# Performance work log

Measured on AMD Instinct MI355X. Metric: run time of the kernel, lower is better.

Reference implementation:

```python
import jax, jax.numpy as jnp
import numpy as np

B, N, K, CIN, COUT, H = 4, 2048, 32, 16, 32, 32
EPS = 1e-5


def setup_inputs() -> dict:
    key = jax.random.key(0)
    ks = jax.random.split(key, 6)
    s = 0.1
    return dict(
        xyz=jax.random.uniform(ks[0], (B, N, 3), dtype=jnp.float32),
        points=jax.random.normal(ks[1], (B, N, CIN), dtype=jnp.float32),
        W1=jax.random.normal(ks[2], (3, H), dtype=jnp.float32) * s,
        b1=jnp.zeros((H,), jnp.float32),
        g1=jnp.ones((H,), jnp.float32),
        be1=jnp.zeros((H,), jnp.float32),
        W2=jax.random.normal(ks[3], (H, H), dtype=jnp.float32) * s,
        b2=jnp.zeros((H,), jnp.float32),
        g2=jnp.ones((H,), jnp.float32),
        be2=jnp.zeros((H,), jnp.float32),
        W3=jax.random.normal(ks[4], (H, CIN * COUT), dtype=jnp.float32) * s,
        b3=jnp.zeros((CIN * COUT,), jnp.float32),
        gbn=jnp.ones((COUT,), jnp.float32),
        bbn=jnp.zeros((COUT,), jnp.float32),
    )


def _bn(h, g, b):
    # BatchNorm1d training-mode math: biased batch stats over axis 0
    return g * (h - h.mean(0)) / jnp.sqrt(h.var(0) + EPS) + b


def reference(xyz, points, W1, b1, g1, be1, W2, b2, g2, be2, W3, b3, gbn, bbn):
    # KNN: squared distances (B,N,N)
    sq = jnp.sum(xyz * xyz, -1)
    dist = -2.0 * jnp.einsum('bmc,bnc->bmn', xyz, xyz) + sq[:, :, None] + sq[:, None, :]
    _, idx = jax.lax.top_k(-dist, K)  # (B,N,K) nearest neighbors

    gather = jax.vmap(lambda p, i: p[i])  # (N,C),(N,K)->(N,K,C), vmapped over B
    grouped_xyz = gather(xyz, idx)                      # (B,N,K,3)
    rel = grouped_xyz - xyz[:, :, None, :]              # (B,N,K,3)
    grouped_pts = gather(points, idx)                   # (B,N,K,CIN)

    # weight net on relative coords
    h = rel.reshape(-1, 3)
    h = _bn(jax.nn.relu(h @ W1 + b1), g1, be1)
    h = _bn(jax.nn.relu(h @ W2 + b2), g2, be2)
    w = (h @ W3 + b3).reshape(B, N, K, CIN, COUT)       # (B,N,K,CIN,COUT)

    # weighted sum over C_in, then max over neighbors
    out = jnp.einsum('bnkc,bnkco->bnko', grouped_pts, w)  # (B,N,K,COUT)
    out = out.max(axis=2)                                 # (B,N,COUT)

    # final BatchNorm1d over (B,N) per channel
    m = out.mean((0, 1))
    v = out.var((0, 1))
    return gbn * (out - m) / jnp.sqrt(v + EPS) + bbn
```

## Files before the change

### kernel.cpp

```cpp
#include <hip/hip_runtime.h>

#define B_ 4
#define N_ 2048
#define K_ 32
#define CIN_ 16
#define COUT_ 32
#define H_ 32
#define R_ (B_*N_*K_)
#define EPS_ 1e-5f
#define INVR_ (1.0f/(float)R_)
#define INVBN_ (1.0f/(float)(B_*N_))
#define LISTCAP 112
#define NSH 16

typedef __attribute__((ext_vector_type(8)))  _Float16 f16x8;
typedef __attribute__((ext_vector_type(2)))  __fp16   hw16x2;
typedef __attribute__((ext_vector_type(2)))  _Float16 f16x2;
typedef __attribute__((ext_vector_type(16))) float    f32x16;

__device__ __forceinline__ float dot3f(float ax,float ay,float az,float bx,float by,float bz){
    return fmaf(az,bz, fmaf(ay,by, ax*bx));
}
__device__ __forceinline__ unsigned int pk2(float a, float b){
    union { hw16x2 v; unsigned int u; } c;
    c.v = __builtin_amdgcn_cvt_pkrtz(a, b);
    return c.u;
}
__device__ __forceinline__ unsigned int pkmul(unsigned int a, unsigned int b){
    union { unsigned int u; f16x2 v; } x, y, r;
    x.u = a; y.u = b; r.v = x.v * y.v; return r.u;
}
__device__ __forceinline__ float shsum(const float* __restrict__ p, int k){
    float s = 0.f;
    #pragma unroll
    for (int i = 0; i < NSH; ++i) s += p[i*32 + k];
    return s;
}

__global__ __launch_bounds__(256) void k_prep0(const float* __restrict__ xyz, float4* __restrict__ xs4g,
                                               float* __restrict__ st){
    int i = blockIdx.x*256 + threadIdx.x;
    float x = xyz[3*i], y = xyz[3*i+1], z = xyz[3*i+2];
    xs4g[i] = make_float4(x, y, z, dot3f(x,y,z,x,y,z));
    if (blockIdx.x == 0){
        for (int j = threadIdx.x; j < 1152; j += 256) st[j] = 0.f;
    }
}

__global__ __launch_bounds__(256,6) void k_knn(const float4* __restrict__ xs4g,
                                               const float* __restrict__ W1, const float* __restrict__ b1,
                                               int* __restrict__ idx_out,
                                               float* __restrict__ s1sh, float* __restrict__ q1sh){
    __shared__ unsigned int hist[4][512][2];
    __shared__ unsigned long long lst[4][LISTCAP];
    __shared__ int kidx[4][K_];

    const int tid  = threadIdx.x;
    const int w    = tid >> 6;
    const int lane = tid & 63;
    const int half = lane >> 5;
    const int b    = blockIdx.x >> 9;
    const int q    = ((blockIdx.x & 511) << 2) + w;
    const int bN   = b * N_;
    unsigned int* hw = &hist[w][0][0];

    const uint4 z4 = make_uint4(0,0,0,0);
    uint4* h4 = (uint4*)hw;
    #pragma unroll
    for (int i = 0; i < 4; ++i) h4[i*64 + lane] = z4;

    const float4 qp = xs4g[bN + q];
    const float qx = qp.x, qy = qp.y, qz = qp.z, sqq = qp.w;

    unsigned int fv[32];
    #pragma unroll
    for (int j = 0; j < 32; ++j){
        int c = j*64 + lane;
        float4 pt = xs4g[bN + c];
        float d = fmaf(-2.0f, dot3f(qx,qy,qz, pt.x,pt.y,pt.z), sqq) + pt.w;
        fv[j] = __float_as_uint(d);
        unsigned int u1 = __float_as_uint(d + 1.0f);
        unsigned int key = (u1 <= 0x3F800000u) ? 0u : ((u1 - 0x3F800000u) >> 15);
        key = key > 511u ? 511u : key;
        atomicAdd(&hw[key*2 + (lane & 1)], 1u);
    }

    unsigned int g[8];
    #pragma unroll
    for (int t = 0; t < 4; ++t){
        uint4 h = ((const uint4*)hw)[lane*4 + t];
        g[2*t]   = h.x + h.y;
        g[2*t+1] = h.z + h.w;
    }
    unsigned int gs = 0;
    #pragma unroll
    for (int t = 0; t < 8; ++t) gs += g[t];
    unsigned int cum = gs;
    #pragma unroll
    for (int off = 1; off < 64; off <<= 1){
        unsigned int v = __shfl_up(cum, off);
        if (lane >= off) cum += v;
    }
    unsigned long long bal = __ballot(cum >= (unsigned)K_);
    int L = __ffsll(bal) - 1;
    unsigned int run = __shfl(cum, L) - __shfl(gs, L);
    int Bsel = 8*L + 7;
    {
        unsigned int c = run; bool fnd = false;
        #pragma unroll
        for (int t = 0; t < 8; ++t){
            unsigned int ht = __shfl(g[t], L, 64);
            if (!fnd && c + ht >= (unsigned)K_){ Bsel = 8*L + t; fnd = true; }
            c += ht;
        }
    }
    const float Tedge = __uint_as_float(0x3F800000u + ((unsigned)(Bsel + 1) << 15));
    const bool allin = (Bsel == 511);

    const unsigned long long mlt = (lane == 63) ? ~0ull >> 1 : (1ull << lane) - 1ull;
    unsigned int cnt = 0;
    #pragma unroll
    for (int j = 0; j < 32; ++j){
        float f1 = __uint_as_float(fv[j]) + 1.0f;
        bool surv = (f1 < Tedge) || allin;
        unsigned long long sb = __ballot(surv);
        unsigned int pos = cnt + (unsigned int)__popcll(sb & mlt);
        if (surv && pos < (unsigned)LISTCAP)
            lst[w][pos] = ((unsigned long long)fv[j] << 32) | (unsigned int)(j*64 + lane);
        cnt += (unsigned int)__popcll(sb);
    }
    int m = (int)cnt; if (m > LISTCAP) m = LISTCAP;

    int* outp = idx_out + ((size_t)bN + q) * K_;
    for (int i = lane; i < m; i += 64){
        unsigned long long my = lst[w][i];
        int rank = 0;
        for (int jj = 0; jj < m; ++jj)
            rank += (lst[w][jj] < my) ? 1 : 0;
        if (rank < K_){
            int id = (int)(unsigned int)(my & 0xFFFFFFFFull);
            outp[rank] = id;
            kidx[w][rank] = id;
        }
    }

    {
        const int ch = lane & 31;
        float w1a = W1[ch], w1b = W1[H_+ch], w1c = W1[2*H_+ch], b1c = b1[ch];
        float s = 0.f, qq = 0.f;
        #pragma unroll
        for (int r = 0; r < 16; ++r){
            int idr = kidx[w][half*16 + r];
            float4 pn = xs4g[bN + idr];
            float rx = pn.x - qx, ry = pn.y - qy, rz = pn.z - qz;
            float h = fmaxf(fmaf(rx, w1a, fmaf(ry, w1b, fmaf(rz, w1c, b1c))), 0.0f);
            s += h; qq = fmaf(h, h, qq);
        }
        s  += __shfl_xor(s, 32, 64);
        qq += __shfl_xor(qq, 32, 64);
        if (lane < 32){
            int sh = (blockIdx.x & (NSH-1)) * 32 + ch;
            atomicAdd(&s1sh[sh], s);
            atomicAdd(&q1sh[sh], qq);
        }
    }
}

__device__ __forceinline__ void compute_h1v(const float4* __restrict__ xs4g, const int* __restrict__ idx, int r,
                                            const float* __restrict__ W1, const float* __restrict__ b1, float* h1){
    int b = r >> 16;
    int n = (r >> 5) & (N_-1);
    int id = idx[r];
    float4 pc = xs4g[b*N_ + n];
    float4 pn = xs4g[b*N_ + id];
    float rx = pn.x - pc.x, ry = pn.y - pc.y, rz = pn.z - pc.z;
    #pragma unroll
    for (int j = 0; j < H_; ++j){
        float a = fmaf(rx, W1[j], fmaf(ry, W1[H_+j], fmaf(rz, W1[2*H_+j], b1[j])));
        h1[j] = fmaxf(a, 0.0f);
    }
}

__global__ __launch_bounds__(256) void k_prep2(const float* __restrict__ points,
                                               const float* __restrict__ s1s, const float* __restrict__ q1s,
                                               const float* __restrict__ g1, const float* __restrict__ be1,
                                               const float* __restrict__ W2, const float* __restrict__ b2,
                                               unsigned int* __restrict__ pf16, unsigned int* __restrict__ W2f,
                                               float* __restrict__ b2p){
    int flat = blockIdx.x*256 + threadIdx.x;
    if (flat < 65536){
        pf16[flat] = pk2(points[2*flat], points[2*flat+1]);
    } else if (flat < 66048){
        int d = flat - 65536;
        int jj = d & 3, lane = (d >> 2) & 63, s = d >> 8;
        int col = lane & 31;
        int k0 = s*16 + (lane >> 5)*8 + 2*jj;
        float m0 = shsum(s1s,k0)*INVR_,   v0 = shsum(q1s,k0)*INVR_   - m0*m0;
        float m1 = shsum(s1s,k0+1)*INVR_, v1 = shsum(q1s,k0+1)*INVR_ - m1*m1;
        float a0  = g1[k0]   / sqrtf(v0 + EPS_);
        float a1v = g1[k0+1] / sqrtf(v1 + EPS_);
        W2f[d] = pk2(a0*W2[k0*H_ + col], a1v*W2[(k0+1)*H_ + col]);
    } else if (flat < 66080){
        int col = flat - 66048;
        float acc = b2[col];
        #pragma unroll 4
        for (int h = 0; h < H_; ++h){
            float mm = shsum(s1s,h)*INVR_, vv = shsum(q1s,h)*INVR_ - mm*mm;
            float aa = g1[h] / sqrtf(vv + EPS_);
            float bb = fmaf(-aa, mm, be1[h]);
            acc = fmaf(bb, W2[h*H_ + col], acc);
        }
        b2p[col] = acc;
    }
}

__global__ __launch_bounds__(256,4) void k_h2stats(const float4* __restrict__ xs4g, const int* __restrict__ idx,
                                                   const float* __restrict__ W1, const float* __restrict__ b1,
                                                   const uint4* __restrict__ W2f, const float* __restrict__ b2p,
                                                   float* gsum, float* gsq){
    __shared__ float redS[H_], redQ[H_];
    const int tid = threadIdx.x, lane = tid & 63, w = tid >> 6;
    const int half = lane >> 5, m = lane & 31;
    if (tid < H_){ redS[tid] = 0.f; redQ[tid] = 0.f; }
    __syncthreads();

    int r = blockIdx.x*256 + tid;
    float h1[H_];
    compute_h1v(xs4g, idx, r, W1, b1, h1);
    unsigned int h1p[16];
    #pragma unroll
    for (int i = 0; i < 16; ++i) h1p[i] = pk2(h1[2*i], h1[2*i+1]);

    union { uint4 u4; f16x8 v; } Bf0, Bf1;
    Bf0.u4 = W2f[lane];
    Bf1.u4 = W2f[64 + lane];
    float b2c = b2p[m];

    float s = 0.f, q = 0.f;
    #pragma unroll
    for (int t = 0; t < 2; ++t){
        const int src = t*32 + m;
        union { unsigned int u[4]; f16x8 v; } a0, a1f;
        #pragma unroll
        for (int jj = 0; jj < 4; ++jj){
            unsigned int lo = __shfl(h1p[jj],     src, 64);
            unsigned int hi = __shfl(h1p[4 + jj], src, 64);
            a0.u[jj] = half ? hi : lo;
        }
        #pragma unroll
        for (int jj = 0; jj < 4; ++jj){
            unsigned int lo = __shfl(h1p[8 + jj],  src, 64);
            unsigned int hi = __shfl(h1p[12 + jj], src, 64);
            a1f.u[jj] = half ? hi : lo;
        }
        f32x16 acc;
        #pragma unroll
        for (int i = 0; i < 16; ++i) acc[i] = b2c;
        acc = __builtin_amdgcn_mfma_f32_32x32x16_f16(a0.v,  Bf0.v, acc, 0, 0, 0);
        acc = __builtin_amdgcn_mfma_f32_32x32x16_f16(a1f.v, Bf1.v, acc, 0, 0, 0);
        #pragma unroll
        for (int i = 0; i < 16; ++i){
            float v = fmaxf(acc[i], 0.0f);
            s += v; q = fmaf(v, v, q);
        }
    }
    s += __shfl_xor(s, 32, 64);
    q += __shfl_xor(q, 32, 64);
    if (lane < 32){ atomicAdd(&redS[m], s); atomicAdd(&redQ[m], q); }
    __syncthreads();
    if (tid < H_){ atomicAdd(&gsum[tid], redS[tid]); atomicAdd(&gsq[tid], redQ[tid]); }
}

__global__ __launch_bounds__(256) void k_prep3(const float* __restrict__ W3, const float* __restrict__ b3,
                                               const float* __restrict__ s2, const float* __restrict__ q2,
                                               const float* __restrict__ g2, const float* __restrict__ be2,
                                               unsigned int* __restrict__ W3f){
    int d = blockIdx.x*256 + threadIdx.x;
    int jj = d & 3, lane = (d >> 2) & 63, step = d >> 8;
    int col = lane & 31;
    int off = (lane >> 5)*8 + 2*jj;
    float v0, v1;
    if (step < 32){
        int h = step, c0 = off;
        float mm = s2[h]*INVR_, vv = q2[h]*INVR_ - mm*mm;
        float aa = g2[h] / sqrtf(vv + EPS_);
        v0 = aa * W3[h*512 + c0*COUT_ + col];
        v1 = aa * W3[h*512 + (c0+1)*COUT_ + col];
    } else {
        int c0 = off;
        v0 = b3[c0*COUT_ + col]; v1 = b3[(c0+1)*COUT_ + col];
        #pragma unroll 4
        for (int h = 0; h < H_; ++h){
            float mm = s2[h]*INVR_, vv = q2[h]*INVR_ - mm*mm;
            float aa = g2[h] / sqrtf(vv + EPS_);
            float bb = fmaf(-aa, mm, be2[h]);
            v0 = fmaf(bb, W3[h*512 + c0*COUT_ + col], v0);
            v1 = fmaf(bb, W3[h*512 + (c0+1)*COUT_ + col], v1);
        }
    }
    W3f[d] = pk2(v0, v1);
}

__global__ __launch_bounds__(256,3) void k_out(const float4* __restrict__ xs4g, const int* __restrict__ idx,
                                               const float* __restrict__ W1, const float* __restrict__ b1,
                                               const uint4* __restrict__ W2f, const float* __restrict__ b2p,
                                               const unsigned int* __restrict__ pf16,
                                               const uint4* __restrict__ W3f,
                                               float* __restrict__ out_pre, float* gsum, float* gsq){
    __shared__ float redS[COUT_], redQ[COUT_];
    const int tid = threadIdx.x, lane = tid & 63, w = tid >> 6;
    const int half = lane >> 5, m = lane & 31;
    if (tid < COUT_){ redS[tid] = 0.f; redQ[tid] = 0.f; }
    __syncthreads();

    const int rB = blockIdx.x*256 + w*64;
    int r = blockIdx.x*256 + tid;

    float h1[H_];
    compute_h1v(xs4g, idx, r, W1, b1, h1);
    unsigned int h1p[16];
    #pragma unroll
    for (int i = 0; i < 16; ++i) h1p[i] = pk2(h1[2*i], h1[2*i+1]);

    union { uint4 u4; f16x8 v; } A0, A1;
    A0.u4 = W2f[lane];
    A1.u4 = W2f[64 + lane];
    float b2v[16];
    #pragma unroll
    for (int i = 0; i < 16; ++i) b2v[i] = b2p[(i&3) + 8*(i>>2) + 4*half];

    const uint4* Wf = W3f + lane;

    #pragma unroll
    for (int t = 0; t < 2; ++t){
        const int src = t*32 + m;
        union { unsigned int u[4]; f16x8 v; } B0f, B1f;
        #pragma unroll
        for (int jj = 0; jj < 4; ++jj){
            unsigned int lo = __shfl(h1p[jj],     src, 64);
            unsigned int hi = __shfl(h1p[4 + jj], src, 64);
            B0f.u[jj] = half ? hi : lo;
        }
        #pragma unroll
        for (int jj = 0; jj < 4; ++jj){
            unsigned int lo = __shfl(h1p[8 + jj],  src, 64);
            unsigned int hi = __shfl(h1p[12 + jj], src, 64);
            B1f.u[jj] = half ? hi : lo;
        }
        f32x16 c2;
        #pragma unroll
        for (int i = 0; i < 16; ++i) c2[i] = b2v[i];
        c2 = __builtin_amdgcn_mfma_f32_32x32x16_f16(A0.v, B0f.v, c2, 0, 0, 0);
        c2 = __builtin_amdgcn_mfma_f32_32x32x16_f16(A1.v, B1f.v, c2, 0, 0, 0);

        unsigned int h2p[16];
        #pragma unroll
        for (int p = 0; p < 8; ++p){
            float v0 = fmaxf(c2[2*p],   0.0f);
            float v1 = fmaxf(c2[2*p+1], 0.0f);
            unsigned int ow = pk2(v0, v1);
            unsigned int ot = __shfl_xor(ow, 32, 64);
            int a = p >> 1, bb = p & 1;
            h2p[4*a + 2*half     + bb] = ow;
            h2p[4*a + 2*(1-half) + bb] = ot;
        }

        int row = rB + t*32 + m;
        int bb_ = row >> 16;
        int idr = idx[row];
        const uint4* gpp = (const uint4*)(pf16 + ((size_t)bb_*N_ + idr)*8);
        uint4 ga = gpp[0], gb = gpp[1];
        unsigned int gsel[4];
        gsel[0] = half ? gb.x : ga.x;
        gsel[1] = half ? gb.y : ga.y;
        gsel[2] = half ? gb.z : ga.z;
        gsel[3] = half ? gb.w : ga.w;

        f32x16 acc;
        #pragma unroll
        for (int i = 0; i < 16; ++i) acc[i] = 0.f;
        #pragma unroll
        for (int kb = 0; kb < 32; ++kb){
            unsigned int hr = h2p[kb >> 1];
            unsigned int hd = __builtin_amdgcn_perm(hr, hr, (kb & 1) ? 0x03020302u : 0x01000100u);
            union { unsigned int u[4]; f16x8 v; } af;
            #pragma unroll
            for (int jj = 0; jj < 4; ++jj) af.u[jj] = pkmul(hd, gsel[jj]);
            union { uint4 u4; f16x8 v; } bf; bf.u4 = Wf[kb*64];
            acc = __builtin_amdgcn_mfma_f32_32x32x16_f16(af.v, bf.v, acc, 0, 0, 0);
        }
        {
            union { unsigned int u[4]; f16x8 v; } af;
            #pragma unroll
            for (int jj = 0; jj < 4; ++jj) af.u[jj] = gsel[jj];
            union { uint4 u4; f16x8 v; } bf; bf.u4 = Wf[32*64];
            acc = __builtin_amdgcn_mfma_f32_32x32x16_f16(af.v, bf.v, acc, 0, 0, 0);
        }

        float v = acc[0];
        #pragma unroll
        for (int i = 1; i < 16; ++i) v = fmaxf(v, acc[i]);
        v = fmaxf(v, __shfl_xor(v, 32, 64));
        if (lane < 32){
            int g = blockIdx.x*8 + w*2 + t;
            out_pre[(size_t)g*COUT_ + m] = v;
            atomicAdd(&redS[m], v);
            atomicAdd(&redQ[m], v*v);
        }
    }
    __syncthreads();
    if (tid < COUT_){ atomicAdd(&gsum[tid], redS[tid]); atomicAdd(&gsq[tid], redQ[tid]); }
}

__global__ __launch_bounds__(256) void k_bn(const float* __restrict__ out_pre,
                                            const float* __restrict__ s3, const float* __restrict__ q3,
                                            const float* __restrict__ gbn, const float* __restrict__ bbn,
                                            float* __restrict__ out){
    int i = blockIdx.x*256 + threadIdx.x;
    int o = i & (COUT_-1);
    float mm = s3[o] * INVBN_;
    float vv = q3[o] * INVBN_ - mm*mm;
    float aa = gbn[o] / sqrtf(vv + EPS_);
    out[i] = fmaf(aa, out_pre[i], fmaf(-aa, mm, bbn[o]));
}

extern "C" void kernel_launch(void* const* d_in, const int* in_sizes, int n_in,
                              void* d_out, int out_size, void* d_ws, size_t ws_size,
                              hipStream_t stream){
    const float* xyz    = (const float*)d_in[0];
    const float* points = (const float*)d_in[1];
    const float* W1  = (const float*)d_in[2];
    const float* b1  = (const float*)d_in[3];
    const float* g1  = (const float*)d_in[4];
    const float* be1 = (const float*)d_in[5];
    const float* W2  = (const float*)d_in[6];
    const float* b2  = (const float*)d_in[7];
    const float* g2  = (const float*)d_in[8];
    const float* be2 = (const float*)d_in[9];
    const float* W3  = (const float*)d_in[10];
    const float* b3  = (const float*)d_in[11];
    const float* gbn = (const float*)d_in[12];
    const float* bbn = (const float*)d_in[13];
    float* out = (float*)d_out;

    char* base = (char*)d_ws;
    int*            idx     = (int*)(base + 0);
    float*          out_pre = (float*)(base + 1048576);
    unsigned int*   pf16    = (unsigned int*)(base + 2097152);
    unsigned int*   W3f     = (unsigned int*)(base + 2359296);
    unsigned int*   W2f     = (unsigned int*)(base + 2393088);
    float*          b2p     = (float*)(base + 2395136);
    float*          st      = (float*)(base + 2395264);
    float4*         xs4g    = (float4*)(base + 2399872);
    float *s1s=st, *q1s=st+512, *s2=st+1024, *q2=st+1056, *s3=st+1088, *q3=st+1120;

    hipLaunchKernelGGL(k_prep0,   dim3(32),      dim3(256), 0, stream, xyz, xs4g, st);
    hipLaunchKernelGGL(k_knn,     dim3(B_*N_/4), dim3(256), 0, stream, xs4g, W1, b1, idx, s1s, q1s);
    hipLaunchKernelGGL(k_prep2,   dim3(260),     dim3(256), 0, stream, points, s1s, q1s, g1, be1, W2, b2,
                       pf16, W2f, b2p);
    hipLaunchKernelGGL(k_h2stats, dim3(R_/256),  dim3(256), 0, stream, xs4g, idx, W1, b1,
                       (const uint4*)W2f, b2p, s2, q2);
    hipLaunchKernelGGL(k_prep3,   dim3(33),      dim3(256), 0, stream, W3, b3, s2, q2, g2, be2, W3f);
    hipLaunchKernelGGL(k_out,     dim3(R_/256),  dim3(256), 0, stream, xs4g, idx, W1, b1,
                       (const uint4*)W2f, b2p, pf16, (const uint4*)W3f, out_pre, s3, q3);
    hipLaunchKernelGGL(k_bn,      dim3(B_*N_*COUT_/256), dim3(256), 0, stream, out_pre, s3, q3, gbn, bbn, out);
}
```

Baseline: 176.1 us.

## Fuse all pipeline stages into one cooperative persistent kernel with grid syncs

Replaces the seven separate kernel launches with a single cooperative kernel. Each former kernel becomes a grid-strided phase separated by grid.sync(). The aim is to remove per-launch overhead and inter-kernel gaps, and the small prep kernels now run on the full grid. In exchange it adds six grid-wide barriers. Occupancy is capped by the launch bounds and the union of shared-memory needs, which may slow the heavy KNN and MFMA phases compared with their tuned standalone launches.

```diff
diff --git a/kernel.cpp b/kernel.cpp
--- a/kernel.cpp
+++ b/kernel.cpp
@@ -1,4 +1,7 @@
 #include <hip/hip_runtime.h>
+#include <hip/hip_cooperative_groups.h>
+
+namespace cg = cooperative_groups;
 
 #define B_ 4
 #define N_ 2048
@@ -37,391 +40,398 @@
     return s;
 }
 
-__global__ __launch_bounds__(256) void k_prep0(const float* __restrict__ xyz, float4* __restrict__ xs4g,
-                                               float* __restrict__ st){
-    int i = blockIdx.x*256 + threadIdx.x;
-    float x = xyz[3*i], y = xyz[3*i+1], z = xyz[3*i+2];
-    xs4g[i] = make_float4(x, y, z, dot3f(x,y,z,x,y,z));
-    if (blockIdx.x == 0){
-        for (int j = threadIdx.x; j < 1152; j += 256) st[j] = 0.f;
-    }
-}
-
-__global__ __launch_bounds__(256,6) void k_knn(const float4* __restrict__ xs4g,
-                                               const float* __restrict__ W1, const float* __restrict__ b1,
-                                               int* __restrict__ idx_out,
-                                               float* __restrict__ s1sh, float* __restrict__ q1sh){
-    __shared__ unsigned int hist[4][512][2];
-    __shared__ unsigned long long lst[4][LISTCAP];
-    __shared__ int kidx[4][K_];
+union SharedMem {
+    struct {
+        unsigned int hist[4][512][2];
+        unsigned long long lst[4][LISTCAP];
+        int kidx[4][K_];
+    } knn;
+    struct {
+        float redS[32], redQ[32];
+    } red;
+};
+
+__global__ __launch_bounds__(256,3) void k_mega(
+        const float* __restrict__ xyz, const float* __restrict__ points,
+        const float* __restrict__ W1, const float* __restrict__ b1,
+        const float* __restrict__ g1, const float* __restrict__ be1,
+        const float* __restrict__ W2, const float* __restrict__ b2,
+        const float* __restrict__ g2, const float* __restrict__ be2,
+        const float* __restrict__ W3, const float* __restrict__ b3,
+        const float* __restrict__ gbn, const float* __restrict__ bbn,
+        float* __restrict__ out, char* __restrict__ base)
+{
+    cg::grid_group grid = cg::this_grid();
+
+    int*            idx     = (int*)(base);
+    float*          out_pre = (float*)(base + 1048576);
+    unsigned int*   pf16    = (unsigned int*)(base + 2097152);
+    unsigned int*   W3f     = (unsigned int*)(base + 2359296);
+    float*          st      = (float*)(base + 2393088);
+    float4*         xs4g    = (float4*)(base + 2398208);
+    unsigned int*   W2fg    = (unsigned int*)(base + 2529280);
+    float*          b2pg    = (float*)(base + 2531328);
+    float *s1s = st, *q1s = st+512, *s2 = st+1024, *q2 = st+1056, *s3 = st+1088, *q3 = st+1120;
 
     const int tid  = threadIdx.x;
-    const int w    = tid >> 6;
-    const int lane = tid & 63;
-    const int half = lane >> 5;
-    const int b    = blockIdx.x >> 9;
-    const int q    = ((blockIdx.x & 511) << 2) + w;
-    const int bN   = b * N_;
-    unsigned int* hw = &hist[w][0][0];
-
-    const uint4 z4 = make_uint4(0,0,0,0);
-    uint4* h4 = (uint4*)hw;
-    #pragma unroll
-    for (int i = 0; i < 4; ++i) h4[i*64 + lane] = z4;
-
-    const float4 qp = xs4g[bN + q];
-    const float qx = qp.x, qy = qp.y, qz = qp.z, sqq = qp.w;
-
-    unsigned int fv[32];
-    #pragma unroll
-    for (int j = 0; j < 32; ++j){
-        int c = j*64 + lane;
-        float4 pt = xs4g[bN + c];
-        float d = fmaf(-2.0f, dot3f(qx,qy,qz, pt.x,pt.y,pt.z), sqq) + pt.w;
-        fv[j] = __float_as_uint(d);
-        unsigned int u1 = __float_as_uint(d + 1.0f);
-        unsigned int key = (u1 <= 0x3F800000u) ? 0u : ((u1 - 0x3F800000u) >> 15);
-        key = key > 511u ? 511u : key;
-        atomicAdd(&hw[key*2 + (lane & 1)], 1u);
-    }
-
-    unsigned int g[8];
-    #pragma unroll
-    for (int t = 0; t < 4; ++t){
-        uint4 h = ((const uint4*)hw)[lane*4 + t];
-        g[2*t]   = h.x + h.y;
-        g[2*t+1] = h.z + h.w;
-    }
-    unsigned int gs = 0;
-    #pragma unroll
-    for (int t = 0; t < 8; ++t) gs += g[t];
-    unsigned int cum = gs;
-    #pragma unroll
-    for (int off = 1; off < 64; off <<= 1){
-        unsigned int v = __shfl_up(cum, off);
-        if (lane >= off) cum += v;
-    }
-    unsigned long long bal = __ballot(cum >= (unsigned)K_);
-    int L = __ffsll(bal) - 1;
-    unsigned int run = __shfl(cum, L) - __shfl(gs, L);
-    int Bsel = 8*L + 7;
+    const int blk  = blockIdx.x;
+    const int nb   = gridDim.x;
+    const int nthr = nb * 256;
+    const int lane = tid & 63, w = tid >> 6;
+    const int half = lane >> 5, m = lane & 31;
+
+    __shared__ SharedMem sh;
+
+    for (int i = blk*256 + tid; i < 65536; i += nthr)
+        pf16[i] = pk2(points[2*i], points[2*i+1]);
+    for (int i = blk*256 + tid; i < B_*N_; i += nthr){
+        float x = xyz[3*i], y = xyz[3*i+1], z = xyz[3*i+2];
+        xs4g[i] = make_float4(x, y, z, dot3f(x,y,z,x,y,z));
+    }
+    if (blk == 0) for (int j = tid; j < 1280; j += 256) st[j] = 0.f;
+    grid.sync();
+
     {
-        unsigned int c = run; bool fnd = false;
+        const int nwav = nb * 4;
+        for (int qg = blk*4 + w; qg < B_*N_; qg += nwav){
+            const int b_ = qg >> 11;
+            const int q  = qg & (N_-1);
+            const int bN = b_ * N_;
+            unsigned int* hw = &sh.knn.hist[w][0][0];
+
+            const uint4 z4 = make_uint4(0,0,0,0);
+            uint4* h4 = (uint4*)hw;
+            #pragma unroll
+            for (int i = 0; i < 4; ++i) h4[i*64 + lane] = z4;
+
+            const float4 qp = xs4g[bN + q];
+            const float qx = qp.x, qy = qp.y, qz = qp.z, sqq = qp.w;
+
+            unsigned int fv[32];
+            #pragma unroll
+            for (int j = 0; j < 32; ++j){
+                int c = j*64 + lane;
+                float4 pt = xs4g[bN + c];
+                float d = fmaf(-2.0f, dot3f(qx,qy,qz, pt.x,pt.y,pt.z), sqq) + pt.w;
+                fv[j] = __float_as_uint(d);
+                unsigned int u1 = __float_as_uint(d + 1.0f);
+                unsigned int key = (u1 <= 0x3F800000u) ? 0u : ((u1 - 0x3F800000u) >> 15);
+                key = key > 511u ? 511u : key;
+                atomicAdd(&hw[key*2 + (lane & 1)], 1u);
+            }
+
+            unsigned int g[8];
+            #pragma unroll
+            for (int t = 0; t < 4; ++t){
+                uint4 h = ((const uint4*)hw)[lane*4 + t];
+                g[2*t]   = h.x + h.y;
+                g[2*t+1] = h.z + h.w;
+            }
+            unsigned int gs = 0;
+            #pragma unroll
+            for (int t = 0; t < 8; ++t) gs += g[t];
+            unsigned int cum = gs;
+            #pragma unroll
+            for (int off = 1; off < 64; off <<= 1){
+                unsigned int v = __shfl_up(cum, off);
+                if (lane >= off) cum += v;
+            }
+            unsigned long long bal = __ballot(cum >= (unsigned)K_);
+            int L = __ffsll(bal) - 1;
+            unsigned int run = __shfl(cum, L) - __shfl(gs, L);
+            int Bsel = 8*L + 7;
+            {
+                unsigned int c = run; bool fnd = false;
+                #pragma unroll
+                for (int t = 0; t < 8; ++t){
+                    unsigned int ht = __shfl(g[t], L, 64);
+                    if (!fnd && c + ht >= (unsigned)K_){ Bsel = 8*L + t; fnd = true; }
+                    c += ht;
+                }
+            }
+            const float Tedge = __uint_as_float(0x3F800000u + ((unsigned)(Bsel + 1) << 15));
+            const bool allin = (Bsel == 511);
+
+            const unsigned long long mlt = (lane == 63) ? ~0ull >> 1 : (1ull << lane) - 1ull;
+            unsigned int cnt = 0;
+            #pragma unroll
+            for (int j = 0; j < 32; ++j){
+                float f1 = __uint_as_float(fv[j]) + 1.0f;
+                bool surv = (f1 < Tedge) || allin;
+                unsigned long long sb = __ballot(surv);
+                unsigned int pos = cnt + (unsigned int)__popcll(sb & mlt);
+                if (surv && pos < (unsigned)LISTCAP)
+                    sh.knn.lst[w][pos] = ((unsigned long long)fv[j] << 32) | (unsigned int)(j*64 + lane);
+                cnt += (unsigned int)__popcll(sb);
+            }
+            int mc = (int)cnt; if (mc > LISTCAP) mc = LISTCAP;
+
+            int* outp = idx + ((size_t)bN + q) * K_;
+            for (int i = lane; i < mc; i += 64){
+                unsigned long long my = sh.knn.lst[w][i];
+                int rank = 0;
+                for (int jj = 0; jj < mc; ++jj)
+                    rank += (sh.knn.lst[w][jj] < my) ? 1 : 0;
+                if (rank < K_){
+                    int id = (int)(unsigned int)(my & 0xFFFFFFFFull);
+                    outp[rank] = id;
+                    sh.knn.kidx[w][rank] = id;
+                }
+            }
+
+            {
+                const int ch = lane & 31;
+                float w1a = W1[ch], w1b = W1[H_+ch], w1c = W1[2*H_+ch], b1c = b1[ch];
+                float s = 0.f, qq = 0.f;
+                #pragma unroll
+                for (int r = 0; r < 16; ++r){
+                    int idr = sh.knn.kidx[w][half*16 + r];
+                    float4 pn = xs4g[bN + idr];
+                    float rx = pn.x - qx, ry = pn.y - qy, rz = pn.z - qz;
+                    float h = fmaxf(fmaf(rx, w1a, fmaf(ry, w1b, fmaf(rz, w1c, b1c))), 0.0f);
+                    s += h; qq = fmaf(h, h, qq);
+                }
+                s  += __shfl_xor(s, 32, 64);
+                qq += __shfl_xor(qq, 32, 64);
+                if (lane < 32){
+                    int shh = (qg & (NSH-1)) * 32 + ch;
+                    atomicAdd(&s1s[shh], s);
+                    atomicAdd(&q1s[shh], qq);
+                }
+            }
+        }
+    }
+    grid.sync();
+
+    for (int t = blk*256 + tid; t < 544; t += nthr){
+        if (t < 512){
+            int d = t, jj = d & 3, ln = (d >> 2) & 63, s = d >> 8;
+            int col = ln & 31;
+            int k0 = s*16 + (ln >> 5)*8 + 2*jj;
+            float m0 = shsum(s1s,k0)*INVR_,   v0 = shsum(q1s,k0)*INVR_   - m0*m0;
+            float m1 = shsum(s1s,k0+1)*INVR_, v1 = shsum(q1s,k0+1)*INVR_ - m1*m1;
+            float a0  = g1[k0]   / sqrtf(v0 + EPS_);
+            float a1v = g1[k0+1] / sqrtf(v1 + EPS_);
+            W2fg[d] = pk2(a0*W2[k0*H_ + col], a1v*W2[(k0+1)*H_ + col]);
+        } else {
+            int col = t - 512;
+            float acc = b2[col];
+            #pragma unroll 4
+            for (int h = 0; h < H_; ++h){
+                float mm = shsum(s1s,h)*INVR_, vv = shsum(q1s,h)*INVR_ - mm*mm;
+                float aa = g1[h] / sqrtf(vv + EPS_);
+                float bb = fmaf(-aa, mm, be1[h]);
+                acc = fmaf(bb, W2[h*H_ + col], acc);
+            }
+            b2pg[col] = acc;
+        }
+    }
+    grid.sync();
+
+    for (int u = blk; u < R_/256; u += nb){
+        if (tid < H_){ sh.red.redS[tid] = 0.f; sh.red.redQ[tid] = 0.f; }
+        __syncthreads();
+
+        int r = u*256 + tid;
+        float h1[H_];
+        {
+            int b_ = r >> 16, n = (r >> 5) & (N_-1), id = idx[r];
+            float4 pc = xs4g[b_*N_ + n];
+            float4 pn = xs4g[b_*N_ + id];
+            float rx = pn.x - pc.x, ry = pn.y - pc.y, rz = pn.z - pc.z;
+            #pragma unroll
+            for (int j = 0; j < H_; ++j)
+                h1[j] = fmaxf(fmaf(rx, W1[j], fmaf(ry, W1[H_+j], fmaf(rz, W1[2*H_+j], b1[j]))), 0.0f);
+        }
+        unsigned int h1p[16];
         #pragma unroll
-        for (int t = 0; t < 8; ++t){
-            unsigned int ht = __shfl(g[t], L, 64);
-            if (!fnd && c + ht >= (unsigned)K_){ Bsel = 8*L + t; fnd = true; }
-            c += ht;
-        }
-    }
-    const float Tedge = __uint_as_float(0x3F800000u + ((unsigned)(Bsel + 1) << 15));
-    const bool allin = (Bsel == 511);
-
-    const unsigned long long mlt = (lane == 63) ? ~0ull >> 1 : (1ull << lane) - 1ull;
-    unsigned int cnt = 0;
-    #pragma unroll
-    for (int j = 0; j < 32; ++j){
-        float f1 = __uint_as_float(fv[j]) + 1.0f;
-        bool surv = (f1 < Tedge) || allin;
-        unsigned long long sb = __ballot(surv);
-        unsigned int pos = cnt + (unsigned int)__popcll(sb & mlt);
-        if (surv && pos < (unsigned)LISTCAP)
-            lst[w][pos] = ((unsigned long long)fv[j] << 32) | (unsigned int)(j*64 + lane);
-        cnt += (unsigned int)__popcll(sb);
-    }
-    int m = (int)cnt; if (m > LISTCAP) m = LISTCAP;
-
-    int* outp = idx_out + ((size_t)bN + q) * K_;
-    for (int i = lane; i < m; i += 64){
-        unsigned long long my = lst[w][i];
-        int rank = 0;
-        for (int jj = 0; jj < m; ++jj)
-            rank += (lst[w][jj] < my) ? 1 : 0;
-        if (rank < K_){
-            int id = (int)(unsigned int)(my & 0xFFFFFFFFull);
-            outp[rank] = id;
-            kidx[w][rank] = id;
-        }
-    }
+        for (int i = 0; i < 16; ++i) h1p[i] = pk2(h1[2*i], h1[2*i+1]);
+
+        union { uint4 u4; f16x8 v; } Bf0, Bf1;
+        Bf0.u4 = ((const uint4*)W2fg)[lane];
+        Bf1.u4 = ((const uint4*)W2fg)[64 + lane];
+        float b2c = b2pg[m];
+
+        float s = 0.f, q = 0.f;
+        #pragma unroll
+        for (int t = 0; t < 2; ++t){
+            const int src = t*32 + m;
+            union { unsigned int u[4]; f16x8 v; } a0, a1f;
+            #pragma unroll
+            for (int jj = 0; jj < 4; ++jj){
+                unsigned int lo = __shfl(h1p[jj],     src, 64);
+                unsigned int hi = __shfl(h1p[4 + jj], src, 64);
+                a0.u[jj] = half ? hi : lo;
+            }
+            #pragma unroll
+            for (int jj = 0; jj < 4; ++jj){
+                unsigned int lo = __shfl(h1p[8 + jj],  src, 64);
+                unsigned int hi = __shfl(h1p[12 + jj], src, 64);
+                a1f.u[jj] = half ? hi : lo;
+            }
+            f32x16 acc;
+            #pragma unroll
+            for (int i = 0; i < 16; ++i) acc[i] = b2c;
+            acc = __builtin_amdgcn_mfma_f32_32x32x16_f16(a0.v,  Bf0.v, acc, 0, 0, 0);
+            acc = __builtin_amdgcn_mfma_f32_32x32x16_f16(a1f.v, Bf1.v, acc, 0, 0, 0);
+            #pragma unroll
+            for (int i = 0; i < 16; ++i){
+                float v = fmaxf(acc[i], 0.0f);
+                s += v; q = fmaf(v, v, q);
+            }
+        }
+        s += __shfl_xor(s, 32, 64);
+        q += __shfl_xor(q, 32, 64);
+        if (lane < 32){ atomicAdd(&sh.red.redS[m], s); atomicAdd(&sh.red.redQ[m], q); }
+        __syncthreads();
+        if (tid < H_){ atomicAdd(&s2[tid], sh.red.redS[tid]); atomicAdd(&q2[tid], sh.red.redQ[tid]); }
+    }
+    grid.sync();
+
+    for (int d = blk*256 + tid; d < 8448; d += nthr){
+        int jj = d & 3, ln = (d >> 2) & 63, step = d >> 8;
+        int col = ln & 31;
+        int off = (ln >> 5)*8 + 2*jj;
+        float v0, v1;
+        if (step < 32){
+            float mm = s2[step]*INVR_, vv = q2[step]*INVR_ - mm*mm;
+            float aa = g2[step] / sqrtf(vv + EPS_);
+            v0 = aa * W3[step*512 + off*COUT_ + col];
+            v1 = aa * W3[step*512 + (off+1)*COUT_ + col];
+        } else {
+            v0 = b3[off*COUT_ + col]; v1 = b3[(off+1)*COUT_ + col];
+            #pragma unroll 4
+            for (int h = 0; h < H_; ++h){
+                float mm = s2[h]*INVR_, vv = q2[h]*INVR_ - mm*mm;
+                float aa = g2[h] / sqrtf(vv + EPS_);
+                float bb = fmaf(-aa, mm, be2[h]);
+                v0 = fmaf(bb, W3[h*512 + off*COUT_ + col], v0);
+                v1 = fmaf(bb, W3[h*512 + (off+1)*COUT_ + col], v1);
+            }
+        }
+        W3f[d] = pk2(v0, v1);
+    }
+    grid.sync();
 
     {
-        const int ch = lane & 31;
-        float w1a = W1[ch], w1b = W1[H_+ch], w1c = W1[2*H_+ch], b1c = b1[ch];
-        float s = 0.f, qq = 0.f;
+        union { uint4 u4; f16x8 v; } A0, A1;
+        A0.u4 = ((const uint4*)W2fg)[lane];
+        A1.u4 = ((const uint4*)W2fg)[64 + lane];
+        float b2v[16];
         #pragma unroll
-        for (int r = 0; r < 16; ++r){
-            int idr = kidx[w][half*16 + r];
-            float4 pn = xs4g[bN + idr];
-            float rx = pn.x - qx, ry = pn.y - qy, rz = pn.z - qz;
-            float h = fmaxf(fmaf(rx, w1a, fmaf(ry, w1b, fmaf(rz, w1c, b1c))), 0.0f);
-            s += h; qq = fmaf(h, h, qq);
-        }
-        s  += __shfl_xor(s, 32, 64);
-        qq += __shfl_xor(qq, 32, 64);
-        if (lane < 32){
-            int sh = (blockIdx.x & (NSH-1)) * 32 + ch;
-            atomicAdd(&s1sh[sh], s);
-            atomicAdd(&q1sh[sh], qq);
-        }
-    }
-}
-
-__device__ __forceinline__ void compute_h1v(const float4* __restrict__ xs4g, const int* __restrict__ idx, int r,
-                                            const float* __restrict__ W1, const float* __restrict__ b1, float* h1){
-    int b = r >> 16;
-    int n = (r >> 5) & (N_-1);
-    int id = idx[r];
-    float4 pc = xs4g[b*N_ + n];
-    float4 pn = xs4g[b*N_ + id];
-    float rx = pn.x - pc.x, ry = pn.y - pc.y, rz = pn.z - pc.z;
-    #pragma unroll
-    for (int j = 0; j < H_; ++j){
-        float a = fmaf(rx, W1[j], fmaf(ry, W1[H_+j], fmaf(rz, W1[2*H_+j], b1[j])));
-        h1[j] = fmaxf(a, 0.0f);
-    }
-}
-
-__global__ __launch_bounds__(256) void k_prep2(const float* __restrict__ points,
-                                               const float* __restrict__ s1s, const float* __restrict__ q1s,
-                                               const float* __restrict__ g1, const float* __restrict__ be1,
-                                               const float* __restrict__ W2, const float* __restrict__ b2,
-                                               unsigned int* __restrict__ pf16, unsigned int* __restrict__ W2f,
-                                               float* __restrict__ b2p){
-    int flat = blockIdx.x*256 + threadIdx.x;
-    if (flat < 65536){
-        pf16[flat] = pk2(points[2*flat], points[2*flat+1]);
-    } else if (flat < 66048){
-        int d = flat - 65536;
-        int jj = d & 3, lane = (d >> 2) & 63, s = d >> 8;
-        int col = lane & 31;
-        int k0 = s*16 + (lane >> 5)*8 + 2*jj;
-        float m0 = shsum(s1s,k0)*INVR_,   v0 = shsum(q1s,k0)*INVR_   - m0*m0;
-        float m1 = shsum(s1s,k0+1)*INVR_, v1 = shsum(q1s,k0+1)*INVR_ - m1*m1;
-        float a0  = g1[k0]   / sqrtf(v0 + EPS_);
-        float a1v = g1[k0+1] / sqrtf(v1 + EPS_);
-        W2f[d] = pk2(a0*W2[k0*H_ + col], a1v*W2[(k0+1)*H_ + col]);
-    } else if (flat < 66080){
-        int col = flat - 66048;
-        float acc = b2[col];
-        #pragma unroll 4
-        for (int h = 0; h < H_; ++h){
-            float mm = shsum(s1s,h)*INVR_, vv = shsum(q1s,h)*INVR_ - mm*mm;
-            float aa = g1[h] / sqrtf(vv + EPS_);
-            float bb = fmaf(-aa, mm, be1[h]);
-            acc = fmaf(bb, W2[h*H_ + col], acc);
-        }
-        b2p[col] = acc;
-    }
-}
-
-__global__ __launch_bounds__(256,4) void k_h2stats(const float4* __restrict__ xs4g, const int* __restrict__ idx,
-                                                   const float* __restrict__ W1, const float* __restrict__ b1,
-                                                   const uint4* __restrict__ W2f, const float* __restrict__ b2p,
-                                                   float* gsum, float* gsq){
-    __shared__ float redS[H_], redQ[H_];
-    const int tid = threadIdx.x, lane = tid & 63, w = tid >> 6;
-    const int half = lane >> 5, m = lane & 31;
-    if (tid < H_){ redS[tid] = 0.f; redQ[tid] = 0.f; }
-    __syncthreads();
-
-    int r = blockIdx.x*256 + tid;
-    float h1[H_];
-    compute_h1v(xs4g, idx, r, W1, b1, h1);
-    unsigned int h1p[16];
-    #pragma unroll
-    for (int i = 0; i < 16; ++i) h1p[i] = pk2(h1[2*i], h1[2*i+1]);
-
-    union { uint4 u4; f16x8 v; } Bf0, Bf1;
-    Bf0.u4 = W2f[lane];
-    Bf1.u4 = W2f[64 + lane];
-    float b2c = b2p[m];
-
-    float s = 0.f, q = 0.f;
-    #pragma unroll
-    for (int t = 0; t < 2; ++t){
-        const int src = t*32 + m;
-        union { unsigned int u[4]; f16x8 v; } a0, a1f;
-        #pragma unroll
-        for (int jj = 0; jj < 4; ++jj){
-            unsigned int lo = __shfl(h1p[jj],     src, 64);
-            unsigned int hi = __shfl(h1p[4 + jj], src, 64);
-            a0.u[jj] = half ? hi : lo;
-        }
-        #pragma unroll
-        for (int jj = 0; jj < 4; ++jj){
-            unsigned int lo = __shfl(h1p[8 + jj],  src, 64);
-            unsigned int hi = __shfl(h1p[12 + jj], src, 64);
-            a1f.u[jj] = half ? hi : lo;
-        }
-        f32x16 acc;
-        #pragma unroll
-        for (int i = 0; i < 16; ++i) acc[i] = b2c;
-        acc = __builtin_amdgcn_mfma_f32_32x32x16_f16(a0.v,  Bf0.v, acc, 0, 0, 0);
-        acc = __builtin_amdgcn_mfma_f32_32x32x16_f16(a1f.v, Bf1.v, acc, 0, 0, 0);
-        #pragma unroll
-        for (int i = 0; i < 16; ++i){
-            float v = fmaxf(acc[i], 0.0f);
-            s += v; q = fmaf(v, v, q);
-        }
-    }
-    s += __shfl_xor(s, 32, 64);
-    q += __shfl_xor(q, 32, 64);
-    if (lane < 32){ atomicAdd(&redS[m], s); atomicAdd(&redQ[m], q); }
-    __syncthreads();
-    if (tid < H_){ atomicAdd(&gsum[tid], redS[tid]); atomicAdd(&gsq[tid], redQ[tid]); }
-}
-
-__global__ __launch_bounds__(256) void k_prep3(const float* __restrict__ W3, const float* __restrict__ b3,
-                                               const float* __restrict__ s2, const float* __restrict__ q2,
-                                               const float* __restrict__ g2, const float* __restrict__ be2,
-                                               unsigned int* __restrict__ W3f){
-    int d = blockIdx.x*256 + threadIdx.x;
-    int jj = d & 3, lane = (d >> 2) & 63, step = d >> 8;
-    int col = lane & 31;
-    int off = (lane >> 5)*8 + 2*jj;
-    float v0, v1;
-    if (step < 32){
-        int h = step, c0 = off;
-        float mm = s2[h]*INVR_, vv = q2[h]*INVR_ - mm*mm;
-        float aa = g2[h] / sqrtf(vv + EPS_);
-        v0 = aa * W3[h*512 + c0*COUT_ + col];
-        v1 = aa * W3[h*512 + (c0+1)*COUT_ + col];
-    } else {
-        int c0 = off;
-        v0 = b3[c0*COUT_ + col]; v1 = b3[(c0+1)*COUT_ + col];
-        #pragma unroll 4
-        for (int h = 0; h < H_; ++h){
-            float mm = s2[h]*INVR_, vv = q2[h]*INVR_ - mm*mm;
-            float aa = g2[h] / sqrtf(vv + EPS_);
-            float bb = fmaf(-aa, mm, be2[h]);
-            v0 = fmaf(bb, W3[h*512 + c0*COUT_ + col], v0);
-            v1 = fmaf(bb, W3[h*512 + (c0+1)*COUT_ + col], v1);
-        }
-    }
-    W3f[d] = pk2(v0, v1);
-}
-
-__global__ __launch_bounds__(256,3) void k_out(const float4* __restrict__ xs4g, const int* __restrict__ idx,
-                                               const float* __restrict__ W1, const float* __restrict__ b1,
-                                               const uint4* __restrict__ W2f, const float* __restrict__ b2p,
-                                               const unsigned int* __restrict__ pf16,
-                                               const uint4* __restrict__ W3f,
-                                               float* __restrict__ out_pre, float* gsum, float* gsq){
-    __shared__ float redS[COUT_], redQ[COUT_];
-    const int tid = threadIdx.x, lane = tid & 63, w = tid >> 6;
-    const int half = lane >> 5, m = lane & 31;
-    if (tid < COUT_){ redS[tid] = 0.f; redQ[tid] = 0.f; }
-    __syncthreads();
-
-    const int rB = blockIdx.x*256 + w*64;
-    int r = blockIdx.x*256 + tid;
-
-    float h1[H_];
-    compute_h1v(xs4g, idx, r, W1, b1, h1);
-    unsigned int h1p[16];
-    #pragma unroll
-    for (int i = 0; i < 16; ++i) h1p[i] = pk2(h1[2*i], h1[2*i+1]);
-
-    union { uint4 u4; f16x8 v; } A0, A1;
-    A0.u4 = W2f[lane];
-    A1.u4 = W2f[64 + lane];
-    float b2v[16];
-    #pragma unroll
-    for (int i = 0; i < 16; ++i) b2v[i] = b2p[(i&3) + 8*(i>>2) + 4*half];
-
-    const uint4* Wf = W3f + lane;
-
-    #pragma unroll
-    for (int t = 0; t < 2; ++t){
-        const int src = t*32 + m;
-        union { unsigned int u[4]; f16x8 v; } B0f, B1f;
-        #pragma unroll
-        for (int jj = 0; jj < 4; ++jj){
-            unsigned int lo = __shfl(h1p[jj],     src, 64);
-            unsigned int hi = __shfl(h1p[4 + jj], src, 64);
-            B0f.u[jj] = half ? hi : lo;
-        }
-        #pragma unroll
-        for (int jj = 0; jj < 4; ++jj){
-            unsigned int lo = __shfl(h1p[8 + jj],  src, 64);
-            unsigned int hi = __shfl(h1p[12 + jj], src, 64);
-            B1f.u[jj] = half ? hi : lo;
-        }
-        f32x16 c2;
-        #pragma unroll
-        for (int i = 0; i < 16; ++i) c2[i] = b2v[i];
-        c2 = __builtin_amdgcn_mfma_f32_32x32x16_f16(A0.v, B0f.v, c2, 0, 0, 0);
-        c2 = __builtin_amdgcn_mfma_f32_32x32x16_f16(A1.v, B1f.v, c2, 0, 0, 0);
-
-        unsigned int h2p[16];
-        #pragma unroll
-        for (int p = 0; p < 8; ++p){
-            float v0 = fmaxf(c2[2*p],   0.0f);
-            float v1 = fmaxf(c2[2*p+1], 0.0f);
-            unsigned int ow = pk2(v0, v1);
-            unsigned int ot = __shfl_xor(ow, 32, 64);
-            int a = p >> 1, bb = p & 1;
-            h2p[4*a + 2*half     + bb] = ow;
-            h2p[4*a + 2*(1-half) + bb] = ot;
-        }
-
-        int row = rB + t*32 + m;
-        int bb_ = row >> 16;
-        int idr = idx[row];
-        const uint4* gpp = (const uint4*)(pf16 + ((size_t)bb_*N_ + idr)*8);
-        uint4 ga = gpp[0], gb = gpp[1];
-        unsigned int gsel[4];
-        gsel[0] = half ? gb.x : ga.x;
-        gsel[1] = half ? gb.y : ga.y;
-        gsel[2] = half ? gb.z : ga.z;
-        gsel[3] = half ? gb.w : ga.w;
-
-        f32x16 acc;
-        #pragma unroll
-        for (int i = 0; i < 16; ++i) acc[i] = 0.f;
-        #pragma unroll
-        for (int kb = 0; kb < 32; ++kb){
-            unsigned int hr = h2p[kb >> 1];
-            unsigned int hd = __builtin_amdgcn_perm(hr, hr, (kb & 1) ? 0x03020302u : 0x01000100u);
-            union { unsigned int u[4]; f16x8 v; } af;
-            #pragma unroll
-            for (int jj = 0; jj < 4; ++jj) af.u[jj] = pkmul(hd, gsel[jj]);
-            union { uint4 u4; f16x8 v; } bf; bf.u4 = Wf[kb*64];
-            acc = __builtin_amdgcn_mfma_f32_32x32x16_f16(af.v, bf.v, acc, 0, 0, 0);
-        }
-        {
-            union { unsigned int u[4]; f16x8 v; } af;
-            #pragma unroll
-            for (int jj = 0; jj < 4; ++jj) af.u[jj] = gsel[jj];
-            union { uint4 u4; f16x8 v; } bf; bf.u4 = Wf[32*64];
-            acc = __builtin_amdgcn_mfma_f32_32x32x16_f16(af.v, bf.v, acc, 0, 0, 0);
-        }
-
-        float v = acc[0];
-        #pragma unroll
-        for (int i = 1; i < 16; ++i) v = fmaxf(v, acc[i]);
-        v = fmaxf(v, __shfl_xor(v, 32, 64));
-        if (lane < 32){
-            int g = blockIdx.x*8 + w*2 + t;
-            out_pre[(size_t)g*COUT_ + m] = v;
-            atomicAdd(&redS[m], v);
-            atomicAdd(&redQ[m], v*v);
-        }
-    }
-    __syncthreads();
-    if (tid < COUT_){ atomicAdd(&gsum[tid], redS[tid]); atomicAdd(&gsq[tid], redQ[tid]); }
-}
-
-__global__ __launch_bounds__(256) void k_bn(const float* __restrict__ out_pre,
-                                            const float* __restrict__ s3, const float* __restrict__ q3,
-                                            const float* __restrict__ gbn, const float* __restrict__ bbn,
-                                            float* __restrict__ out){
-    int i = blockIdx.x*256 + threadIdx.x;
-    int o = i & (COUT_-1);
-    float mm = s3[o] * INVBN_;
-    float vv = q3[o] * INVBN_ - mm*mm;
-    float aa = gbn[o] / sqrtf(vv + EPS_);
-    out[i] = fmaf(aa, out_pre[i], fmaf(-aa, mm, bbn[o]));
+        for (int i = 0; i < 16; ++i) b2v[i] = b2pg[(i&3) + 8*(i>>2) + 4*half];
+        const uint4* Wf = (const uint4*)W3f + lane;
+
+        for (int u = blk; u < R_/256; u += nb){
+            if (tid < COUT_){ sh.red.redS[tid] = 0.f; sh.red.redQ[tid] = 0.f; }
+            __syncthreads();
+
+            const int rB = u*256 + w*64;
+            int r = u*256 + tid;
+            float h1[H_];
+            {
+                int b_ = r >> 16, n = (r >> 5) & (N_-1), id = idx[r];
+                float4 pc = xs4g[b_*N_ + n];
+                float4 pn = xs4g[b_*N_ + id];
+                float rx = pn.x - pc.x, ry = pn.y - pc.y, rz = pn.z - pc.z;
+                #pragma unroll
+                for (int j = 0; j < H_; ++j)
+                    h1[j] = fmaxf(fmaf(rx, W1[j], fmaf(ry, W1[H_+j], fmaf(rz, W1[2*H_+j], b1[j]))), 0.0f);
+            }
+            unsigned int h1p[16];
+            #pragma unroll
+            for (int i = 0; i < 16; ++i) h1p[i] = pk2(h1[2*i], h1[2*i+1]);
+
+            #pragma unroll
+            for (int t = 0; t < 2; ++t){
+                const int src = t*32 + m;
+                union { unsigned int u[4]; f16x8 v; } B0f, B1f;
+                #pragma unroll
+                for (int jj = 0; jj < 4; ++jj){
+                    unsigned int lo = __shfl(h1p[jj],     src, 64);
+                    unsigned int hi = __shfl(h1p[4 + jj], src, 64);
+                    B0f.u[jj] = half ? hi : lo;
+                }
+                #pragma unroll
+                for (int jj = 0; jj < 4; ++jj){
+                    unsigned int lo = __shfl(h1p[8 + jj],  src, 64);
+                    unsigned int hi = __shfl(h1p[12 + jj], src, 64);
+                    B1f.u[jj] = half ? hi : lo;
+                }
+                f32x16 c2;
+                #pragma unroll
+                for (int i = 0; i < 16; ++i) c2[i] = b2v[i];
+                c2 = __builtin_amdgcn_mfma_f32_32x32x16_f16(A0.v, B0f.v, c2, 0, 0, 0);
+                c2 = __builtin_amdgcn_mfma_f32_32x32x16_f16(A1.v, B1f.v, c2, 0, 0, 0);
+
+                unsigned int h2p[16];
+                #pragma unroll
+                for (int p = 0; p < 8; ++p){
+                    float v0 = fmaxf(c2[2*p],   0.0f);
+                    float v1 = fmaxf(c2[2*p+1], 0.0f);
+                    unsigned int ow = pk2(v0, v1);
+                    unsigned int ot = __shfl_xor(ow, 32, 64);
+                    int a = p >> 1, bb = p & 1;
+                    h2p[4*a + 2*half     + bb] = ow;
+                    h2p[4*a + 2*(1-half) + bb] = ot;
+                }
+
+                int row = rB + t*32 + m;
+                int bb_ = row >> 16;
+                int idr = idx[row];
+                const uint4* gpp = (const uint4*)(pf16 + ((size_t)bb_*N_ + idr)*8);
+                uint4 ga = gpp[0], gb = gpp[1];
+                unsigned int gsel[4];
+                gsel[0] = half ? gb.x : ga.x;
+                gsel[1] = half ? gb.y : ga.y;
+                gsel[2] = half ? gb.z : ga.z;
+                gsel[3] = half ? gb.w : ga.w;
+
+                f32x16 acc;
+                #pragma unroll
+                for (int i = 0; i < 16; ++i) acc[i] = 0.f;
+                #pragma unroll
+                for (int kb = 0; kb < 32; ++kb){
+                    unsigned int hr = h2p[kb >> 1];
+                    unsigned int hd = __builtin_amdgcn_perm(hr, hr, (kb & 1) ? 0x03020302u : 0x01000100u);
+                    union { unsigned int u[4]; f16x8 v; } af;
+                    #pragma unroll
+                    for (int jj = 0; jj < 4; ++jj) af.u[jj] = pkmul(hd, gsel[jj]);
+                    union { uint4 u4; f16x8 v; } bf; bf.u4 = Wf[kb*64];
+                    acc = __builtin_amdgcn_mfma_f32_32x32x16_f16(af.v, bf.v, acc, 0, 0, 0);
+                }
+                {
+                    union { unsigned int u[4]; f16x8 v; } af;
+                    #pragma unroll
+                    for (int jj = 0; jj < 4; ++jj) af.u[jj] = gsel[jj];
+                    union { uint4 u4; f16x8 v; } bf; bf.u4 = Wf[32*64];
+                    acc = __builtin_amdgcn_mfma_f32_32x32x16_f16(af.v, bf.v, acc, 0, 0, 0);
+                }
+
+                float v = acc[0];
+                #pragma unroll
+                for (int i = 1; i < 16; ++i) v = fmaxf(v, acc[i]);
+                v = fmaxf(v, __shfl_xor(v, 32, 64));
+                if (lane < 32){
+                    int gidx = u*8 + w*2 + t;
+                    out_pre[(size_t)gidx*COUT_ + m] = v;
+                    atomicAdd(&sh.red.redS[m], v);
+                    atomicAdd(&sh.red.redQ[m], v*v);
+                }
+            }
+            __syncthreads();
+            if (tid < COUT_){ atomicAdd(&s3[tid], sh.red.redS[tid]); atomicAdd(&q3[tid], sh.red.redQ[tid]); }
+        }
+    }
+    grid.sync();
+
+    for (int i = blk*256 + tid; i < B_*N_*COUT_; i += nthr){
+        int o = i & (COUT_-1);
+        float mm = s3[o] * INVBN_;
+        float vv = q3[o] * INVBN_ - mm*mm;
+        float aa = gbn[o] / sqrtf(vv + EPS_);
+        out[i] = fmaf(aa, out_pre[i], fmaf(-aa, mm, bbn[o]));
+    }
 }
 
 extern "C" void kernel_launch(void* const* d_in, const int* in_sizes, int n_in,
@@ -442,26 +452,18 @@
     const float* gbn = (const float*)d_in[12];
     const float* bbn = (const float*)d_in[13];
     float* out = (float*)d_out;
-
     char* base = (char*)d_ws;
-    int*            idx     = (int*)(base + 0);
-    float*          out_pre = (float*)(base + 1048576);
-    unsigned int*   pf16    = (unsigned int*)(base + 2097152);
-    unsigned int*   W3f     = (unsigned int*)(base + 2359296);
-    unsigned int*   W2f     = (unsigned int*)(base + 2393088);
-    float*          b2p     = (float*)(base + 2395136);
-    float*          st      = (float*)(base + 2395264);
-    float4*         xs4g    = (float4*)(base + 2399872);
-    float *s1s=st, *q1s=st+512, *s2=st+1024, *q2=st+1056, *s3=st+1088, *q3=st+1120;
-
-    hipLaunchKernelGGL(k_prep0,   dim3(32),      dim3(256), 0, stream, xyz, xs4g, st);
-    hipLaunchKernelGGL(k_knn,     dim3(B_*N_/4), dim3(256), 0, stream, xs4g, W1, b1, idx, s1s, q1s);
-    hipLaunchKernelGGL(k_prep2,   dim3(260),     dim3(256), 0, stream, points, s1s, q1s, g1, be1, W2, b2,
-                       pf16, W2f, b2p);
-    hipLaunchKernelGGL(k_h2stats, dim3(R_/256),  dim3(256), 0, stream, xs4g, idx, W1, b1,
-                       (const uint4*)W2f, b2p, s2, q2);
-    hipLaunchKernelGGL(k_prep3,   dim3(33),      dim3(256), 0, stream, W3, b3, s2, q2, g2, be2, W3f);
-    hipLaunchKernelGGL(k_out,     dim3(R_/256),  dim3(256), 0, stream, xs4g, idx, W1, b1,
-                       (const uint4*)W2f, b2p, pf16, (const uint4*)W3f, out_pre, s3, q3);
-    hipLaunchKernelGGL(k_bn,      dim3(B_*N_*COUT_/256), dim3(256), 0, stream, out_pre, s3, q3, gbn, bbn, out);
-}
+
+    int occ = 0;
+    hipOccupancyMaxActiveBlocksPerMultiprocessor(&occ, k_mega, 256, 0);
+    if (occ < 1) occ = 1;
+    if (occ > 8) occ = 8;
+    dim3 grid(occ * 256), block(256);
+
+    void* args[] = {
+        (void*)&xyz, (void*)&points, (void*)&W1, (void*)&b1, (void*)&g1, (void*)&be1,
+        (void*)&W2, (void*)&b2, (void*)&g2, (void*)&be2, (void*)&W3, (void*)&b3,
+        (void*)&gbn, (void*)&bbn, (void*)&out, (void*)&base
+    };
+    hipLaunchCooperativeKernel(k_mega, grid, block, args, 0, stream);
+}
```

Result: slower. 451.6 us (+156.5%).
